# Optimization experiments

Measured on AMD Instinct MI355X. Metric: run time of the kernel, lower is better.

The kernel has to match this reference:

```python
import jax, jax.numpy as jnp
import numpy as np

DT = 0.001
TAU_MEM = 0.01
TAU_SYN = 0.005
THRESHOLD = 1.0
INITIAL_STATE = 0.0
SS_BETA = 100.0  # SuperSpike surrogate slope (Zenke & Ganguli)


@jax.custom_vjp
def superspike(x):
    # Heaviside spike in forward
    return (x > 0).astype(x.dtype)

def _ss_fwd(x):
    return superspike(x), x

def _ss_bwd(x, g):
    # fast-sigmoid surrogate gradient
    return (g / (SS_BETA * jnp.abs(x) + 1.0) ** 2,)

superspike.defvjp(_ss_fwd, _ss_bwd)


def setup_inputs() -> dict:
    key = jax.random.key(0)
    k1, k2 = jax.random.split(key)
    B, T, IN, OUT = 64, 1024, 256, 256
    inputs = jax.random.normal(k1, (B, T, IN), dtype=jnp.float32)
    w = jax.random.normal(k2, (IN, OUT), dtype=jnp.float32) * 4.0  # scale=4.0 in __init__
    return {"inputs": inputs, "w": w}


def _simulate_mem(inputs, w):
    # inputs: [B, T, IN], w: [IN, OUT]
    x = jnp.matmul(inputs, w)  # [B, T, OUT]
    T = x.shape[1]
    dcy_mem = jnp.exp(jnp.asarray(-DT / (TAU_MEM + 1e-16), dtype=x.dtype))
    scl_mem = 1.0 - dcy_mem
    dcy_syn = jnp.exp(jnp.asarray(-DT / (TAU_SYN + 1e-16), dtype=x.dtype))

    zeros0 = jnp.zeros_like(x[:, 0])  # initial_state = 0

    def step(carry, x_t):
        syn, mem = carry
        new_syn = dcy_syn * syn + x_t
        new_mem = dcy_mem * mem + scl_mem * syn  # uses OLD syn
        out = superspike(mem - THRESHOLD)        # spike from OLD mem
        new_mem = new_mem * (1.0 - out)          # reset
        return (new_syn, new_mem), new_mem

    # loop runs over t = 0 .. T-2 (matches `for t in range(nb_steps - 1)`)
    xs = jnp.swapaxes(x[:, : T - 1], 0, 1)  # [T-1, B, OUT]
    _, mems = jax.lax.scan(step, (zeros0, zeros0), xs)
    mems = jnp.swapaxes(mems, 0, 1)  # [B, T-1, OUT]
    # prepend the initial stored state (zeros, since initial_state=0)
    U = jnp.concatenate([zeros0[:, None, :], mems], axis=1)  # [B, T, OUT]
    return U


def reference(inputs, w):
    # monitor == 'mem' -> return membrane potential trace U
    return _simulate_mem(inputs, w)
```

## Files before the change

kernel.cpp:

```cpp
#include <hip/hip_runtime.h>
#include <cmath>

typedef short bf16x8 __attribute__((ext_vector_type(8)));
typedef float f32x4 __attribute__((ext_vector_type(4)));

#define T_DIM 1024

__device__ __forceinline__ unsigned short rtn_bf16(float f) {
    unsigned u = __float_as_uint(f);
    return (unsigned short)((u + 0x7FFFu + ((u >> 16) & 1u)) >> 16);
}
__device__ __forceinline__ void split3(float f, unsigned short& h1,
                                       unsigned short& h2, unsigned short& h3) {
    unsigned u = __float_as_uint(f);
    h1 = (unsigned short)(u >> 16);
    float r1 = f - __uint_as_float(u & 0xFFFF0000u);
    unsigned u1 = __float_as_uint(r1);
    h2 = (unsigned short)(u1 >> 16);
    float r2 = r1 - __uint_as_float(u1 & 0xFFFF0000u);
    h3 = rtn_bf16(r2);
}

__global__ __launch_bounds__(256) void lif_wsplit(const float* __restrict__ w,
                                                  unsigned short* __restrict__ wT1,
                                                  unsigned short* __restrict__ wT2,
                                                  unsigned short* __restrict__ wT3) {
    const int id = blockIdx.x * 256 + threadIdx.x;
    const int k = id >> 8, n = id & 255;
    unsigned short h1, h2, h3;
    split3(w[id], h1, h2, h3);
    const int o = n * 256 + k;
    wT1[o] = h1; wT2[o] = h2; wT3[o] = h3;
}

__global__ __launch_bounds__(256) void lif_gemm_mfma(const float* __restrict__ in,
                                                     const unsigned short* __restrict__ wT1,
                                                     const unsigned short* __restrict__ wT2,
                                                     const unsigned short* __restrict__ wT3,
                                                     float* __restrict__ xbuf) {
    const int tid  = threadIdx.x;
    const int bm   = blockIdx.x;
    const int bn   = blockIdx.y;
    const int wave = tid >> 6;
    const int lane = tid & 63;
    const int l15  = lane & 15;
    const int quad = lane >> 4;
    const int wm   = (wave >> 1) * 64;
    const int wn   = (wave & 1) * 64;

    f32x4 acc[4][4];
    #pragma unroll
    for (int i = 0; i < 4; ++i)
        #pragma unroll
        for (int j = 0; j < 4; ++j) acc[i][j] = (f32x4){0.f, 0.f, 0.f, 0.f};

    const float* arow0 = in + (size_t)(bm * 128 + wm + l15) * 256 + quad * 8;

    const size_t wrow = (size_t)(bn * 128 + wn + l15) * 256 + quad * 8;

    float4 rv[4][2];
    #pragma unroll
    for (int mt = 0; mt < 4; ++mt) {
        const float* ap = arow0 + mt * 16 * 256;
        rv[mt][0] = *(const float4*)(ap);
        rv[mt][1] = *(const float4*)(ap + 4);
    }

    #pragma unroll 1
    for (int kt = 0; kt < 8; ++kt) {
        const int k0 = kt * 32;

        size_t wo = wrow + k0;
        bf16x8 b1 = *(const bf16x8*)(wT1 + wo);
        bf16x8 b2 = *(const bf16x8*)(wT2 + wo);
        bf16x8 b3 = *(const bf16x8*)(wT3 + wo);

        bf16x8 af[3][4];
        #pragma unroll
        for (int mt = 0; mt < 4; ++mt) {
            const float fv[8] = {rv[mt][0].x, rv[mt][0].y, rv[mt][0].z, rv[mt][0].w,
                                 rv[mt][1].x, rv[mt][1].y, rv[mt][1].z, rv[mt][1].w};
            #pragma unroll
            for (int i = 0; i < 8; ++i) {
                unsigned short h1, h2, h3;
                split3(fv[i], h1, h2, h3);
                af[0][mt][i] = (short)h1;
                af[1][mt][i] = (short)h2;
                af[2][mt][i] = (short)h3;
            }
        }

        if (kt < 7) {
            #pragma unroll
            for (int mt = 0; mt < 4; ++mt) {
                const float* ap = arow0 + mt * 16 * 256 + (k0 + 32);
                rv[mt][0] = *(const float4*)(ap);
                rv[mt][1] = *(const float4*)(ap + 4);
            }
        }

        #pragma unroll
        for (int nt = 0; nt < 4; ++nt) {
            bf16x8 n1, n2, n3;
            if (nt < 3) {
                const size_t won = wo + (size_t)16 * 256;
                n1 = *(const bf16x8*)(wT1 + won);
                n2 = *(const bf16x8*)(wT2 + won);
                n3 = *(const bf16x8*)(wT3 + won);
            }
            #pragma unroll
            for (int mt = 0; mt < 4; ++mt) {
                f32x4 a = acc[mt][nt];
                a = __builtin_amdgcn_mfma_f32_16x16x32_bf16(af[0][mt], b1, a, 0, 0, 0);
                a = __builtin_amdgcn_mfma_f32_16x16x32_bf16(af[0][mt], b2, a, 0, 0, 0);
                a = __builtin_amdgcn_mfma_f32_16x16x32_bf16(af[1][mt], b1, a, 0, 0, 0);
                a = __builtin_amdgcn_mfma_f32_16x16x32_bf16(af[1][mt], b2, a, 0, 0, 0);
                a = __builtin_amdgcn_mfma_f32_16x16x32_bf16(af[0][mt], b3, a, 0, 0, 0);
                a = __builtin_amdgcn_mfma_f32_16x16x32_bf16(af[2][mt], b1, a, 0, 0, 0);
                acc[mt][nt] = a;
            }
            if (nt < 3) { b1 = n1; b2 = n2; b3 = n3; wo += (size_t)16 * 256; }
        }
    }

    #pragma unroll
    for (int mt = 0; mt < 4; ++mt) {
        #pragma unroll
        for (int nt = 0; nt < 4; ++nt) {
            const int C  = bn * 128 + wn + nt * 16 + l15;
            const int Rb = bm * 128 + wm + mt * 16 + quad * 4;
            #pragma unroll
            for (int reg = 0; reg < 4; ++reg)
                xbuf[(size_t)(Rb + reg) * 256 + C] = acc[mt][nt][reg];
        }
    }
}

__global__ __launch_bounds__(64, 1) void lif_scan(const float* __restrict__ xbuf,
                                                  float* __restrict__ U,
                                                  double dcy_syn, double dcy_mem,
                                                  double scl_mem) {
    const int b = blockIdx.x >> 2;
    const int o = (blockIdx.x & 3) * 64 + threadIdx.x;

    const float* xp = xbuf + (size_t)b * T_DIM * 256 + o;
    float* up = U + (size_t)b * T_DIM * 256 + o;

    up[0] = 0.0f;
    double syn = 0.0, mem = 0.0;

    float bufA[64], bufB[64];
    #pragma unroll
    for (int j = 0; j < 64; ++j)
        bufA[j] = xp[(size_t)j * 256];

    #pragma unroll 1
    for (int bt = 0; bt < 8; ++bt) {
        const int tb = bt * 128;
        {
            const float* np = xp + (size_t)(tb + 64) * 256;
            #pragma unroll
            for (int j = 0; j < 64; ++j)
                bufB[j] = np[(size_t)j * 256];
        }
        #pragma unroll
        for (int j = 0; j < 64; ++j) {
            const int t = tb + j;
            double nm = dcy_mem * mem + scl_mem * syn;
            if (mem - 1.0 > 0.0) nm = 0.0;
            syn = dcy_syn * syn + (double)bufA[j];
            mem = nm;
            __builtin_nontemporal_store((float)mem, up + (size_t)(t + 1) * 256);
        }
        if (bt < 7) {
            const float* np = xp + (size_t)(tb + 128) * 256;
            #pragma unroll
            for (int j = 0; j < 64; ++j)
                bufA[j] = np[(size_t)j * 256];
        }
        #pragma unroll
        for (int j = 0; j < 64; ++j) {
            const int t = tb + 64 + j;
            double nm = dcy_mem * mem + scl_mem * syn;
            if (mem - 1.0 > 0.0) nm = 0.0;
            syn = dcy_syn * syn + (double)bufB[j];
            mem = nm;
            if (t < T_DIM - 1)
                __builtin_nontemporal_store((float)mem, up + (size_t)(t + 1) * 256);
        }
    }
}

extern "C" void kernel_launch(void* const* d_in, const int* in_sizes, int n_in,
                              void* d_out, int out_size, void* d_ws, size_t ws_size,
                              hipStream_t stream) {
    const float* in = (const float*)d_in[0];
    const float* w  = (const float*)d_in[1];
    float* U = (float*)d_out;

    const double dcy_mem = exp(-0.001 / (0.01  + 1e-16));
    const double dcy_syn = exp(-0.001 / (0.005 + 1e-16));
    const double scl_mem = 1.0 - dcy_mem;

    char* ws = (char*)d_ws;
    unsigned short* wT1 = (unsigned short*)ws;
    unsigned short* wT2 = (unsigned short*)(ws + 131072);
    unsigned short* wT3 = (unsigned short*)(ws + 262144);
    float* xbuf = (float*)(ws + 524288);

    lif_wsplit<<<dim3(256), dim3(256), 0, stream>>>(w, wT1, wT2, wT3);
    lif_gemm_mfma<<<dim3(512, 2), dim3(256), 0, stream>>>(in, wT1, wT2, wT3, xbuf);
    lif_scan<<<dim3(256), dim3(64), 0, stream>>>(xbuf, U, dcy_syn, dcy_mem, scl_mem);
}
```

Baseline: 212.1 us.

## Fuse GEMM and LIF scan into one kernel with LDS double-buffered time tiles

Replaces the separate GEMM and scan kernels with one fused kernel per (batch, 64-column group). Waves compute 128-timestep GEMM tiles into double-buffered shared memory while one wave scans the previous tile, carrying syn/mem state through LDS. This avoids writing and re-reading the full intermediate activation buffer in global memory and overlaps matmul with the sequential recurrence. In exchange, each block re-reads its batch's inputs for only 64 outputs, so input traffic is quadrupled, and the scan is serialized across waves with block barriers.

Result: slower. 269.8 us (+27.2%).

```diff
diff --git a/kernel.cpp b/kernel.cpp
--- a/kernel.cpp
+++ b/kernel.cpp
@@ -33,53 +33,48 @@
     wT1[o] = h1; wT2[o] = h2; wT3[o] = h3;
 }
 
-__global__ __launch_bounds__(256) void lif_gemm_mfma(const float* __restrict__ in,
-                                                     const unsigned short* __restrict__ wT1,
-                                                     const unsigned short* __restrict__ wT2,
-                                                     const unsigned short* __restrict__ wT3,
-                                                     float* __restrict__ xbuf) {
-    const int tid  = threadIdx.x;
-    const int bm   = blockIdx.x;
-    const int bn   = blockIdx.y;
-    const int wave = tid >> 6;
-    const int lane = tid & 63;
-    const int l15  = lane & 15;
-    const int quad = lane >> 4;
-    const int wm   = (wave >> 1) * 64;
-    const int wn   = (wave & 1) * 64;
-
-    f32x4 acc[4][4];
-    #pragma unroll
-    for (int i = 0; i < 4; ++i)
-        #pragma unroll
-        for (int j = 0; j < 4; ++j) acc[i][j] = (f32x4){0.f, 0.f, 0.f, 0.f};
-
-    const float* arow0 = in + (size_t)(bm * 128 + wm + l15) * 256 + quad * 8;
-
-    const size_t wrow = (size_t)(bn * 128 + wn + l15) * 256 + quad * 8;
-
-    float4 rv[4][2];
-    #pragma unroll
-    for (int mt = 0; mt < 4; ++mt) {
-        const float* ap = arow0 + mt * 16 * 256;
-        rv[mt][0] = *(const float4*)(ap);
-        rv[mt][1] = *(const float4*)(ap + 4);
-    }
-
-    #pragma unroll 1
-    for (int kt = 0; kt < 8; ++kt) {
-        const int k0 = kt * 32;
-
-        size_t wo = wrow + k0;
-        bf16x8 b1 = *(const bf16x8*)(wT1 + wo);
-        bf16x8 b2 = *(const bf16x8*)(wT2 + wo);
-        bf16x8 b3 = *(const bf16x8*)(wT3 + wo);
-
-        bf16x8 af[3][4];
-        #pragma unroll
-        for (int mt = 0; mt < 4; ++mt) {
-            const float fv[8] = {rv[mt][0].x, rv[mt][0].y, rv[mt][0].z, rv[mt][0].w,
-                                 rv[mt][1].x, rv[mt][1].y, rv[mt][1].z, rv[mt][1].w};
+__device__ __forceinline__ void gemm_tile(const float* __restrict__ abase,
+                                          const unsigned short* __restrict__ wT1,
+                                          const unsigned short* __restrict__ wT2,
+                                          const unsigned short* __restrict__ wT3,
+                                          size_t wbase,
+                                          float* __restrict__ xtile,
+                                          int ms, int ns, int l15, int quad) {
+    f32x4 acc[2][2];
+    #pragma unroll
+    for (int i = 0; i < 2; ++i)
+        #pragma unroll
+        for (int j = 0; j < 2; ++j) acc[i][j] = (f32x4){0.f, 0.f, 0.f, 0.f};
+
+    float4 rvP[2][2][2];
+    bf16x8 bv[3][2];
+
+    #pragma unroll
+    for (int mt = 0; mt < 2; ++mt) {
+        const float* ap = abase + (size_t)mt * 16 * 256;
+        rvP[0][mt][0] = *(const float4*)(ap);
+        rvP[0][mt][1] = *(const float4*)(ap + 4);
+        rvP[1][mt][0] = *(const float4*)(ap + 32);
+        rvP[1][mt][1] = *(const float4*)(ap + 36);
+    }
+    #pragma unroll
+    for (int nt = 0; nt < 2; ++nt) {
+        const size_t wo = wbase + (size_t)nt * 16 * 256;
+        bv[0][nt] = *(const bf16x8*)(wT1 + wo);
+        bv[1][nt] = *(const bf16x8*)(wT2 + wo);
+        bv[2][nt] = *(const bf16x8*)(wT3 + wo);
+    }
+
+    #pragma unroll
+    for (int kf = 0; kf < 8; ++kf) {
+        const int par = kf & 1;
+        bf16x8 af[3][2];
+        #pragma unroll
+        for (int mt = 0; mt < 2; ++mt) {
+            const float fv[8] = {rvP[par][mt][0].x, rvP[par][mt][0].y,
+                                 rvP[par][mt][0].z, rvP[par][mt][0].w,
+                                 rvP[par][mt][1].x, rvP[par][mt][1].y,
+                                 rvP[par][mt][1].z, rvP[par][mt][1].w};
             #pragma unroll
             for (int i = 0; i < 8; ++i) {
                 unsigned short h1, h2, h3;
@@ -89,105 +84,135 @@
                 af[2][mt][i] = (short)h3;
             }
         }
-
-        if (kt < 7) {
-            #pragma unroll
-            for (int mt = 0; mt < 4; ++mt) {
-                const float* ap = arow0 + mt * 16 * 256 + (k0 + 32);
-                rv[mt][0] = *(const float4*)(ap);
-                rv[mt][1] = *(const float4*)(ap + 4);
-            }
-        }
-
-        #pragma unroll
-        for (int nt = 0; nt < 4; ++nt) {
-            bf16x8 n1, n2, n3;
-            if (nt < 3) {
-                const size_t won = wo + (size_t)16 * 256;
-                n1 = *(const bf16x8*)(wT1 + won);
-                n2 = *(const bf16x8*)(wT2 + won);
-                n3 = *(const bf16x8*)(wT3 + won);
-            }
-            #pragma unroll
-            for (int mt = 0; mt < 4; ++mt) {
+        bf16x8 cb[3][2];
+        #pragma unroll
+        for (int q = 0; q < 3; ++q) { cb[q][0] = bv[q][0]; cb[q][1] = bv[q][1]; }
+        if (kf < 6) {
+            #pragma unroll
+            for (int mt = 0; mt < 2; ++mt) {
+                const float* ap = abase + (size_t)mt * 16 * 256 + (kf + 2) * 32;
+                rvP[par][mt][0] = *(const float4*)(ap);
+                rvP[par][mt][1] = *(const float4*)(ap + 4);
+            }
+        }
+        if (kf < 7) {
+            #pragma unroll
+            for (int nt = 0; nt < 2; ++nt) {
+                const size_t wo = wbase + (size_t)nt * 16 * 256 + (kf + 1) * 32;
+                bv[0][nt] = *(const bf16x8*)(wT1 + wo);
+                bv[1][nt] = *(const bf16x8*)(wT2 + wo);
+                bv[2][nt] = *(const bf16x8*)(wT3 + wo);
+            }
+        }
+        #pragma unroll
+        for (int nt = 0; nt < 2; ++nt) {
+            #pragma unroll
+            for (int mt = 0; mt < 2; ++mt) {
                 f32x4 a = acc[mt][nt];
-                a = __builtin_amdgcn_mfma_f32_16x16x32_bf16(af[0][mt], b1, a, 0, 0, 0);
-                a = __builtin_amdgcn_mfma_f32_16x16x32_bf16(af[0][mt], b2, a, 0, 0, 0);
-                a = __builtin_amdgcn_mfma_f32_16x16x32_bf16(af[1][mt], b1, a, 0, 0, 0);
-                a = __builtin_amdgcn_mfma_f32_16x16x32_bf16(af[1][mt], b2, a, 0, 0, 0);
-                a = __builtin_amdgcn_mfma_f32_16x16x32_bf16(af[0][mt], b3, a, 0, 0, 0);
-                a = __builtin_amdgcn_mfma_f32_16x16x32_bf16(af[2][mt], b1, a, 0, 0, 0);
+                a = __builtin_amdgcn_mfma_f32_16x16x32_bf16(af[0][mt], cb[0][nt], a, 0, 0, 0);
+                a = __builtin_amdgcn_mfma_f32_16x16x32_bf16(af[0][mt], cb[1][nt], a, 0, 0, 0);
+                a = __builtin_amdgcn_mfma_f32_16x16x32_bf16(af[1][mt], cb[0][nt], a, 0, 0, 0);
+                a = __builtin_amdgcn_mfma_f32_16x16x32_bf16(af[1][mt], cb[1][nt], a, 0, 0, 0);
+                a = __builtin_amdgcn_mfma_f32_16x16x32_bf16(af[0][mt], cb[2][nt], a, 0, 0, 0);
+                a = __builtin_amdgcn_mfma_f32_16x16x32_bf16(af[2][mt], cb[0][nt], a, 0, 0, 0);
                 acc[mt][nt] = a;
             }
-            if (nt < 3) { b1 = n1; b2 = n2; b3 = n3; wo += (size_t)16 * 256; }
-        }
-    }
-
-    #pragma unroll
-    for (int mt = 0; mt < 4; ++mt) {
-        #pragma unroll
-        for (int nt = 0; nt < 4; ++nt) {
-            const int C  = bn * 128 + wn + nt * 16 + l15;
-            const int Rb = bm * 128 + wm + mt * 16 + quad * 4;
+        }
+    }
+
+    #pragma unroll
+    for (int mt = 0; mt < 2; ++mt)
+        #pragma unroll
+        for (int nt = 0; nt < 2; ++nt) {
+            const int c  = ns * 32 + nt * 16 + l15;
+            const int r0 = ms * 32 + mt * 16 + quad * 4;
             #pragma unroll
             for (int reg = 0; reg < 4; ++reg)
-                xbuf[(size_t)(Rb + reg) * 256 + C] = acc[mt][nt][reg];
-        }
-    }
-}
-
-__global__ __launch_bounds__(64, 1) void lif_scan(const float* __restrict__ xbuf,
-                                                  float* __restrict__ U,
-                                                  double dcy_syn, double dcy_mem,
-                                                  double scl_mem) {
-    const int b = blockIdx.x >> 2;
-    const int o = (blockIdx.x & 3) * 64 + threadIdx.x;
-
-    const float* xp = xbuf + (size_t)b * T_DIM * 256 + o;
-    float* up = U + (size_t)b * T_DIM * 256 + o;
-
-    up[0] = 0.0f;
-    double syn = 0.0, mem = 0.0;
-
-    float bufA[64], bufB[64];
-    #pragma unroll
-    for (int j = 0; j < 64; ++j)
-        bufA[j] = xp[(size_t)j * 256];
+                xtile[(r0 + reg) * 64 + c] = acc[mt][nt][reg];
+        }
+}
+
+__global__ __launch_bounds__(512) void lif_fused(const float* __restrict__ in,
+                                                 const unsigned short* __restrict__ wT1,
+                                                 const unsigned short* __restrict__ wT2,
+                                                 const unsigned short* __restrict__ wT3,
+                                                 float* __restrict__ U,
+                                                 double dcy_syn, double dcy_mem,
+                                                 double scl_mem) {
+    __shared__ float  xs[2][128 * 64];
+    __shared__ double stS[64], stM[64];
+
+    const int tid  = threadIdx.x;
+    const int blk  = blockIdx.x;
+    const int b    = blk >> 2;
+    const int og   = (blk & 3) * 64;
+    const int w    = tid >> 6;
+    const int lane = tid & 63;
+    const int l15  = lane & 15;
+    const int quad = lane >> 4;
+    const int ms   = w >> 1;
+    const int ns   = w & 1;
+
+    if (tid < 64) {
+        stS[tid] = 0.0; stM[tid] = 0.0;
+        U[(size_t)b * T_DIM * 256 + og + tid] = 0.0f;
+    }
+
+    const float* abase = in + ((size_t)b * 1024 + ms * 32 + l15) * 256 + quad * 8;
+    const size_t wbase = (size_t)(og + ns * 32 + l15) * 256 + quad * 8;
+
+    gemm_tile(abase, wT1, wT2, wT3, wbase, xs[0], ms, ns, l15, quad);
+    __syncthreads();
 
     #pragma unroll 1
-    for (int bt = 0; bt < 8; ++bt) {
-        const int tb = bt * 128;
-        {
-            const float* np = xp + (size_t)(tb + 64) * 256;
-            #pragma unroll
-            for (int j = 0; j < 64; ++j)
-                bufB[j] = np[(size_t)j * 256];
-        }
-        #pragma unroll
-        for (int j = 0; j < 64; ++j) {
-            const int t = tb + j;
-            double nm = dcy_mem * mem + scl_mem * syn;
-            if (mem - 1.0 > 0.0) nm = 0.0;
-            syn = dcy_syn * syn + (double)bufA[j];
-            mem = nm;
-            __builtin_nontemporal_store((float)mem, up + (size_t)(t + 1) * 256);
-        }
-        if (bt < 7) {
-            const float* np = xp + (size_t)(tb + 128) * 256;
-            #pragma unroll
-            for (int j = 0; j < 64; ++j)
-                bufA[j] = np[(size_t)j * 256];
-        }
-        #pragma unroll
-        for (int j = 0; j < 64; ++j) {
-            const int t = tb + 64 + j;
-            double nm = dcy_mem * mem + scl_mem * syn;
-            if (mem - 1.0 > 0.0) nm = 0.0;
-            syn = dcy_syn * syn + (double)bufB[j];
-            mem = nm;
-            if (t < T_DIM - 1)
-                __builtin_nontemporal_store((float)mem, up + (size_t)(t + 1) * 256);
-        }
+    for (int i = 0; i < 8; ++i) {
+        if (i < 7)
+            gemm_tile(abase + (size_t)(i + 1) * 128 * 256, wT1, wT2, wT3, wbase,
+                      xs[(i + 1) & 1], ms, ns, l15, quad);
+
+        if (w == i) {
+            double syn = stS[lane], mem = stM[lane];
+            const float* xb = &xs[i & 1][0] + lane;
+            float* uo = U + (size_t)b * T_DIM * 256 + og + lane;
+            const int t0 = i * 128;
+
+            float xwA[8], xwB[8];
+            #pragma unroll
+            for (int j = 0; j < 8; ++j) xwA[j] = xb[j * 64];
+
+            #pragma unroll 1
+            for (int cc = 0; cc < 8; ++cc) {
+                const int tb = t0 + cc * 16;
+                #pragma unroll
+                for (int j = 0; j < 8; ++j) xwB[j] = xb[(cc * 16 + 8 + j) * 64];
+                #pragma unroll
+                for (int j = 0; j < 8; ++j) {
+                    const int t = tb + j;
+                    double nm = dcy_mem * mem + scl_mem * syn;
+                    if (mem - 1.0 > 0.0) nm = 0.0;
+                    syn = dcy_syn * syn + (double)xwA[j];
+                    mem = nm;
+                    if (t < T_DIM - 1)
+                        __builtin_nontemporal_store((float)mem, uo + (size_t)(t + 1) * 256);
+                }
+                if (cc < 7) {
+                    #pragma unroll
+                    for (int j = 0; j < 8; ++j) xwA[j] = xb[(cc * 16 + 16 + j) * 64];
+                }
+                #pragma unroll
+                for (int j = 0; j < 8; ++j) {
+                    const int t = tb + 8 + j;
+                    double nm = dcy_mem * mem + scl_mem * syn;
+                    if (mem - 1.0 > 0.0) nm = 0.0;
+                    syn = dcy_syn * syn + (double)xwB[j];
+                    mem = nm;
+                    if (t < T_DIM - 1)
+                        __builtin_nontemporal_store((float)mem, uo + (size_t)(t + 1) * 256);
+                }
+            }
+            stS[lane] = syn; stM[lane] = mem;
+        }
+        __syncthreads();
     }
 }
 
@@ -206,9 +231,8 @@
     unsigned short* wT1 = (unsigned short*)ws;
     unsigned short* wT2 = (unsigned short*)(ws + 131072);
     unsigned short* wT3 = (unsigned short*)(ws + 262144);
-    float* xbuf = (float*)(ws + 524288);
 
     lif_wsplit<<<dim3(256), dim3(256), 0, stream>>>(w, wT1, wT2, wT3);
-    lif_gemm_mfma<<<dim3(512, 2), dim3(256), 0, stream>>>(in, wT1, wT2, wT3, xbuf);
-    lif_scan<<<dim3(256), dim3(64), 0, stream>>>(xbuf, U, dcy_syn, dcy_mem, scl_mem);
-}
+    lif_fused<<<dim3(256), dim3(512), 0, stream>>>(in, wT1, wT2, wT3, U,
+                                                   dcy_syn, dcy_mem, scl_mem);
+}
```
